# Kernel tuning notes

Hardware: AMD Instinct MI355X
Metric: run time of the kernel (lower is better)

The kernel has to match this reference:

```python
import jax, jax.numpy as jnp
import numpy as np

N_NODES = 100000
N_EDGES = 1000000
IN_DIM = 64
HID = 64
OUT = 64
NEG_SLOPE = 0.2  # PyG GATConv default


def setup_inputs() -> dict:
    key = jax.random.key(0)
    ks = jax.random.split(key, 10)
    x = jax.random.normal(ks[0], (N_NODES, IN_DIM), dtype=jnp.float32)
    edge_index = jax.random.randint(ks[1], (2, N_EDGES), 0, N_NODES, dtype=jnp.int64)
    s = 1.0 / np.sqrt(IN_DIM)
    sh = 1.0 / np.sqrt(HID)
    W_src = jax.random.uniform(ks[2], (IN_DIM, HID), jnp.float32, -s, s)
    W_dst = jax.random.uniform(ks[3], (IN_DIM, HID), jnp.float32, -s, s)
    att_src = jax.random.uniform(ks[4], (HID,), jnp.float32, -sh, sh)
    att_dst = jax.random.uniform(ks[5], (HID,), jnp.float32, -sh, sh)
    bias = jnp.zeros((HID,), jnp.float32)
    W_lin = jax.random.uniform(ks[6], (HID, OUT), jnp.float32, -sh, sh)
    b_lin = jax.random.uniform(ks[7], (OUT,), jnp.float32, -sh, sh)
    return {"x": x, "edge_index": edge_index, "W_src": W_src, "W_dst": W_dst,
            "att_src": att_src, "att_dst": att_dst, "bias": bias,
            "W_lin": W_lin, "b_lin": b_lin}


def reference(x, edge_index, W_src, W_dst, att_src, att_dst, bias, W_lin, b_lin):
    src, tgt = edge_index[0], edge_index[1]
    # Bias-free linear projections (PyG GATConv with tuple in_channels)
    h_src = x @ W_src                      # [N, HID]
    h_dst = x @ W_dst                      # [N, HID]
    a_src = h_src @ att_src                # [N]
    a_dst = h_dst @ att_dst                # [N]
    # Per-edge attention logits: LeakyReLU(a_src[j] + a_dst[i])
    e = a_src[src] + a_dst[tgt]            # [E]
    e = jnp.where(e > 0, e, NEG_SLOPE * e)
    # Segment-softmax over incoming edges of each target node
    seg_max = jax.ops.segment_max(e, tgt, num_segments=N_NODES)  # [N]
    expw = jnp.exp(e - seg_max[tgt])                             # [E]
    denom = jax.ops.segment_sum(expw, tgt, num_segments=N_NODES)  # [N]
    alpha = expw / (denom[tgt] + 1e-16)                          # [E]
    # Scatter-aggregate weighted source features
    msgs = alpha[:, None] * h_src[src]                           # [E, HID]
    out = jax.ops.segment_sum(msgs, tgt, num_segments=N_NODES)   # [N, HID]
    out = out + bias
    # Final linear + ReLU
    return jax.nn.relu(out @ W_lin + b_lin)
```

## Files before the change

kernel.cpp:

```cpp
#include <hip/hip_runtime.h>
#include <hip/hip_fp16.h>
#include <math.h>

#define HID 64
#define CBITS 6
#define CSZ 64
#define MAXB 2048
#define CAP 832
#define CAPH 576
#define PB 896
#define MSB 256

__device__ __forceinline__ float4 f4fma(float a, const float4 b, float4 c) {
    c.x = fmaf(a, b.x, c.x); c.y = fmaf(a, b.y, c.y);
    c.z = fmaf(a, b.z, c.z); c.w = fmaf(a, b.w, c.w);
    return c;
}

__global__ void init_kernel(const float* __restrict__ W_dst,
                            const float* __restrict__ att_dst,
                            float* __restrict__ vdst,
                            int* __restrict__ gcursor, int nbc) {
    if (blockIdx.x == 0 && threadIdx.x < HID) {
        int k = threadIdx.x;
        float acc = 0.0f;
#pragma unroll 8
        for (int h = 0; h < HID; ++h) acc = fmaf(W_dst[k * HID + h], att_dst[h], acc);
        vdst[k] = acc;
    }
    int stride = gridDim.x * blockDim.x;
    for (int i = blockIdx.x * blockDim.x + threadIdx.x; i < nbc; i += stride)
        gcursor[i] = i * CAP;
}

__global__ void __launch_bounds__(256)
mid_kernel(const float* __restrict__ x,
           const float* __restrict__ W_src,
           const float* __restrict__ att_src,
           const float* __restrict__ vdst,
           __half* __restrict__ h_half,
           float* __restrict__ a_src,
           float* __restrict__ a_dst, int N,
           const int* __restrict__ src, const int* __restrict__ tgt,
           int* __restrict__ gcursor, int* __restrict__ rec, int E, int nbc) {
    __shared__ __align__(16) char smraw[25088];
    const int t = threadIdx.x;

    if (blockIdx.x < PB) {
        float4* Ws4  = (float4*)smraw;
        float4* att4 = Ws4 + HID * 16;
        float4* vd4  = att4 + 16;
        float*  xs   = (float*)(vd4 + 16);

        for (int i = t; i < HID * 16; i += 256) Ws4[i] = ((const float4*)W_src)[i];
        if (t < 16) {
            att4[t] = ((const float4*)att_src)[t];
            vd4[t]  = ((const float4*)vdst)[t];
        }

        const int g0 = t >> 4;
        const int s = t & 15;
        const float4* x4 = (const float4*)x;
        uint2* h2 = (uint2*)h_half;
        float4* xs4 = (float4*)xs;

        for (int base = blockIdx.x * 32; base < N; base += PB * 32) {
            __syncthreads();
#pragma unroll
            for (int u = 0; u < 2; ++u) {
                int f = t + u * 256;
                int node = base + (f >> 4);
                xs4[f] = (node < N) ? x4[(long long)node * 16 + (f & 15)]
                                    : make_float4(0, 0, 0, 0);
            }
            __syncthreads();

            const float* xr0 = xs + g0 * HID;
            const float* xr1 = xs + (g0 + 16) * HID;

            float4 acc0 = make_float4(0, 0, 0, 0);
            float4 acc1 = make_float4(0, 0, 0, 0);
#pragma unroll 4
            for (int k = 0; k < HID; ++k) {
                float4 w = Ws4[k * 16 + s];
                acc0 = f4fma(xr0[k], w, acc0);
                acc1 = f4fma(xr1[k], w, acc1);
            }

            float4 av = att4[s], qv = vd4[s];
            float p0 = acc0.x * av.x + acc0.y * av.y + acc0.z * av.z + acc0.w * av.w;
            float p1 = acc1.x * av.x + acc1.y * av.y + acc1.z * av.z + acc1.w * av.w;
            float q0 = xr0[4 * s] * qv.x + xr0[4 * s + 1] * qv.y +
                       xr0[4 * s + 2] * qv.z + xr0[4 * s + 3] * qv.w;
            float q1 = xr1[4 * s] * qv.x + xr1[4 * s + 1] * qv.y +
                       xr1[4 * s + 2] * qv.z + xr1[4 * s + 3] * qv.w;
#pragma unroll
            for (int off = 1; off < 16; off <<= 1) {
                p0 += __shfl_xor(p0, off, 64);
                p1 += __shfl_xor(p1, off, 64);
                q0 += __shfl_xor(q0, off, 64);
                q1 += __shfl_xor(q1, off, 64);
            }

            int n0 = base + g0, n1 = base + g0 + 16;
            if (n0 < N) {
                __half2 lo = __float22half2_rn(make_float2(acc0.x, acc0.y));
                __half2 hi = __float22half2_rn(make_float2(acc0.z, acc0.w));
                uint2 pk; pk.x = *(unsigned*)&lo; pk.y = *(unsigned*)&hi;
                h2[(long long)n0 * 16 + s] = pk;
                if (s == 0) { a_src[n0] = p0; a_dst[n0] = q0; }
            }
            if (n1 < N) {
                __half2 lo = __float22half2_rn(make_float2(acc1.x, acc1.y));
                __half2 hi = __float22half2_rn(make_float2(acc1.z, acc1.w));
                uint2 pk; pk.x = *(unsigned*)&lo; pk.y = *(unsigned*)&hi;
                h2[(long long)n1 * 16 + s] = pk;
                if (s == 0) { a_src[n1] = p1; a_dst[n1] = q1; }
            }
        }
    } else {
        int* lh = (int*)smraw;
        const int bid = blockIdx.x - PB;

        for (int i = t; i < nbc; i += 256) lh[i] = 0;
        __syncthreads();
        int chunk = (E + MSB - 1) / MSB;
        int e0 = bid * chunk;
        int e1 = min(E, e0 + chunk);
        for (int e = e0 + t; e < e1; e += 256)
            atomicAdd(&lh[tgt[e] >> CBITS], 1);
        __syncthreads();
        for (int i = t; i < nbc; i += 256)
            if (lh[i]) lh[i] = atomicAdd(&gcursor[i], lh[i]);
        __syncthreads();
        for (int e = e0 + t; e < e1; e += 256) {
            int s = src[e], tg = tgt[e];
            int bi = tg >> CBITS;
            int pos = atomicAdd(&lh[bi], 1);
            if (pos < (bi + 1) * CAP)
                rec[pos] = (s << CBITS) | (tg & (CSZ - 1));
        }
    }
}

__global__ void __launch_bounds__(256)
sort_gather_kernel(const int* __restrict__ gcursor, const int* __restrict__ rec,
                   const __half* __restrict__ h_half,
                   const float* __restrict__ a_src, const float* __restrict__ a_dst,
                   const float* __restrict__ bias,
                   const float* __restrict__ W_lin, const float* __restrict__ b_lin,
                   float* __restrict__ out, int N) {
    __shared__ float4 Wl4[HID * 16];
    __shared__ float4 bs4[16], bl4[16];
    __shared__ int ssort[CAPH];
    __shared__ int hist[32];
    __shared__ int loff[33];
    __shared__ int cur[32];
    __shared__ int sd[32];

    const int t = threadIdx.x;
    for (int i = t; i < HID * 16; i += 256) Wl4[i] = ((const float4*)W_lin)[i];
    if (t < 16) {
        bs4[t] = ((const float4*)bias)[t];
        bl4[t] = ((const float4*)b_lin)[t];
    }

    const int bk = blockIdx.x >> 1;
    const int half = blockIdx.x & 1;
    const int node0 = (bk << CBITS) + half * 32;
    const int nn = min(32, N - node0);
    const int beg = bk * CAP;
    int cnt = gcursor[bk] - beg;
    if (cnt > CAP) cnt = CAP;

    if (t < 32) hist[t] = 0;
    __syncthreads();
    for (int j = t; j < cnt; j += 256) {
        int tl = rec[beg + j] & (CSZ - 1);
        if ((tl >> 5) == half) atomicAdd(&hist[tl & 31], 1);
    }
    __syncthreads();
    if (t < 32) sd[t] = hist[t];
    __syncthreads();
    for (int off = 1; off < 32; off <<= 1) {
        int v = (t < 32 && t >= off) ? sd[t - off] : 0;
        __syncthreads();
        if (t < 32) sd[t] += v;
        __syncthreads();
    }
    if (t < 32) {
        int e = sd[t] - hist[t];
        loff[t] = e; cur[t] = e;
        if (t == 31) loff[32] = min(sd[31], CAPH);
    }
    __syncthreads();
    for (int j = t; j < cnt; j += 256) {
        int r = rec[beg + j];
        int tl = r & (CSZ - 1);
        if ((tl >> 5) == half) {
            int pos = atomicAdd(&cur[tl & 31], 1);
            if (pos < CAPH) ssort[pos] = r >> CBITS;
        }
    }
    __syncthreads();

    const int lane = t & 63;
    const int w = t >> 6;
    const int g = lane >> 4;
    const int s = lane & 15;
    const int gbase = g << 4;
    const uint2* h2 = (const uint2*)h_half;
    float4* out4 = (float4*)out;

#pragma unroll 1
    for (int r2 = 0; r2 < 2; ++r2) {
        int nloc = w * 8 + r2 * 4 + g;
        int n = node0 + nloc;
        bool act = (nloc < nn);
        float adn = act ? a_dst[n] : 0.0f;
        int jb = min(loff[nloc], CAPH);
        int je = min(loff[nloc + 1], CAPH);

        float4 acc = make_float4(0, 0, 0, 0);
        float dsum = 0.0f;
        int j = jb;
        for (; j + 4 <= je; j += 4) {
            int s0 = ssort[j], s1 = ssort[j + 1], s2 = ssort[j + 2], s3 = ssort[j + 3];
            uint2 r0 = h2[(long long)s0 * 16 + s];
            uint2 r1 = h2[(long long)s1 * 16 + s];
            uint2 r2v = h2[(long long)s2 * 16 + s];
            uint2 r3 = h2[(long long)s3 * 16 + s];
            float v0 = a_src[s0] + adn, v1 = a_src[s1] + adn;
            float v2 = a_src[s2] + adn, v3 = a_src[s3] + adn;
            v0 = (v0 > 0.0f) ? v0 : 0.2f * v0;
            v1 = (v1 > 0.0f) ? v1 : 0.2f * v1;
            v2 = (v2 > 0.0f) ? v2 : 0.2f * v2;
            v3 = (v3 > 0.0f) ? v3 : 0.2f * v3;
            float w0 = __expf(v0), w1 = __expf(v1);
            float w2 = __expf(v2), w3 = __expf(v3);
            dsum += (w0 + w1) + (w2 + w3);
            float2 f0a = __half22float2(*(const __half2*)&r0.x);
            float2 f0b = __half22float2(*(const __half2*)&r0.y);
            float2 f1a = __half22float2(*(const __half2*)&r1.x);
            float2 f1b = __half22float2(*(const __half2*)&r1.y);
            float2 f2a = __half22float2(*(const __half2*)&r2v.x);
            float2 f2b = __half22float2(*(const __half2*)&r2v.y);
            float2 f3a = __half22float2(*(const __half2*)&r3.x);
            float2 f3b = __half22float2(*(const __half2*)&r3.y);
            acc.x = fmaf(w0, f0a.x, fmaf(w1, f1a.x, fmaf(w2, f2a.x, fmaf(w3, f3a.x, acc.x))));
            acc.y = fmaf(w0, f0a.y, fmaf(w1, f1a.y, fmaf(w2, f2a.y, fmaf(w3, f3a.y, acc.y))));
            acc.z = fmaf(w0, f0b.x, fmaf(w1, f1b.x, fmaf(w2, f2b.x, fmaf(w3, f3b.x, acc.z))));
            acc.w = fmaf(w0, f0b.y, fmaf(w1, f1b.y, fmaf(w2, f2b.y, fmaf(w3, f3b.y, acc.w))));
        }
        for (; j < je; ++j) {
            int s0 = ssort[j];
            uint2 r0 = h2[(long long)s0 * 16 + s];
            float v0 = a_src[s0] + adn;
            v0 = (v0 > 0.0f) ? v0 : 0.2f * v0;
            float w0 = __expf(v0);
            dsum += w0;
            float2 f0a = __half22float2(*(const __half2*)&r0.x);
            float2 f0b = __half22float2(*(const __half2*)&r0.y);
            acc.x = fmaf(w0, f0a.x, acc.x);
            acc.y = fmaf(w0, f0a.y, acc.y);
            acc.z = fmaf(w0, f0b.x, acc.z);
            acc.w = fmaf(w0, f0b.y, acc.w);
        }

        float inv = 1.0f / (dsum + 1e-16f);
        float4 bsv = bs4[s];
        float4 r;
        r.x = fmaf(acc.x, inv, bsv.x);
        r.y = fmaf(acc.y, inv, bsv.y);
        r.z = fmaf(acc.z, inv, bsv.z);
        r.w = fmaf(acc.w, inv, bsv.w);

        float4 o = bl4[s];
#pragma unroll 4
        for (int ks = 0; ks < 16; ++ks) {
            float rx = __shfl(r.x, gbase + ks, 64);
            float ry = __shfl(r.y, gbase + ks, 64);
            float rz = __shfl(r.z, gbase + ks, 64);
            float rw = __shfl(r.w, gbase + ks, 64);
            o = f4fma(rx, Wl4[(4 * ks + 0) * 16 + s], o);
            o = f4fma(ry, Wl4[(4 * ks + 1) * 16 + s], o);
            o = f4fma(rz, Wl4[(4 * ks + 2) * 16 + s], o);
            o = f4fma(rw, Wl4[(4 * ks + 3) * 16 + s], o);
        }

        if (act) {
            float4 res;
            res.x = o.x > 0.0f ? o.x : 0.0f;
            res.y = o.y > 0.0f ? o.y : 0.0f;
            res.z = o.z > 0.0f ? o.z : 0.0f;
            res.w = o.w > 0.0f ? o.w : 0.0f;
            out4[(long long)n * 16 + s] = res;
        }
    }
}

extern "C" void kernel_launch(void* const* d_in, const int* in_sizes, int n_in,
                              void* d_out, int out_size, void* d_ws, size_t ws_size,
                              hipStream_t stream) {
    const float* x       = (const float*)d_in[0];
    const int*   edge    = (const int*)d_in[1];
    const float* W_src   = (const float*)d_in[2];
    const float* W_dst   = (const float*)d_in[3];
    const float* att_src = (const float*)d_in[4];
    const float* att_dst = (const float*)d_in[5];
    const float* bias    = (const float*)d_in[6];
    const float* W_lin   = (const float*)d_in[7];
    const float* b_lin   = (const float*)d_in[8];
    float* out = (float*)d_out;

    const int N = in_sizes[0] / HID;
    const int E = in_sizes[1] / 2;
    const int* src = edge;
    const int* tgt = edge + E;
    const int nbc = (N + CSZ - 1) / CSZ;

    __half* h_half  = (__half*)d_ws;
    float*  a_src   = (float*)(h_half + (size_t)N * HID);
    float*  a_dst   = a_src + N;
    float*  vdst    = a_dst + N;
    int*    gcursor = (int*)(vdst + 64);
    int*    rec     = gcursor + MAXB;

    init_kernel<<<8, 256, 0, stream>>>(W_dst, att_dst, vdst, gcursor, nbc);
    mid_kernel<<<PB + MSB, 256, 0, stream>>>(x, W_src, att_src, vdst, h_half,
                                             a_src, a_dst, N,
                                             src, tgt, gcursor, rec, E, nbc);
    sort_gather_kernel<<<nbc * 2, 256, 0, stream>>>(gcursor, rec, h_half, a_src, a_dst,
                                                    bias, W_lin, b_lin, out, N);
}
```

Baseline: 164.3 us.

## Replace per-node sort with LDS atomic accumulation over unsorted bucket edges

The gather stage no longer sorts each bucket's edges by target node. One 512-thread block per 64-node bucket now walks the unsorted edge records and adds weighted features and exp sums into a shared-memory accumulator with atomics. This removes the histogram, prefix-scan and scatter passes and their barriers, and lets reads of the record array be vectorised. The cost is many shared-memory float atomics, with possible contention when several edges hit the same target. The W_src layout in mid_kernel is also permuted to match a strided column order.

New measurement: 527.6 us. 221% more time.

```diff
diff --git a/kernel.cpp b/kernel.cpp
--- a/kernel.cpp
+++ b/kernel.cpp
@@ -7,7 +7,6 @@
 #define CSZ 64
 #define MAXB 2048
 #define CAP 832
-#define CAPH 576
 #define PB 896
 #define MSB 256
 
@@ -52,9 +51,14 @@
         float4* vd4  = att4 + 16;
         float*  xs   = (float*)(vd4 + 16);
 
-        for (int i = t; i < HID * 16; i += 256) Ws4[i] = ((const float4*)W_src)[i];
+        for (int i = t; i < HID * 16; i += 256) {
+            int k = i >> 4, sc = i & 15;
+            const float* wr = W_src + k * HID + sc;
+            Ws4[i] = make_float4(wr[0], wr[16], wr[32], wr[48]);
+        }
         if (t < 16) {
-            att4[t] = ((const float4*)att_src)[t];
+            att4[t] = make_float4(att_src[t], att_src[t + 16],
+                                  att_src[t + 32], att_src[t + 48]);
             vd4[t]  = ((const float4*)vdst)[t];
         }
 
@@ -143,131 +147,131 @@
     }
 }
 
-__global__ void __launch_bounds__(256)
-sort_gather_kernel(const int* __restrict__ gcursor, const int* __restrict__ rec,
-                   const __half* __restrict__ h_half,
-                   const float* __restrict__ a_src, const float* __restrict__ a_dst,
-                   const float* __restrict__ bias,
-                   const float* __restrict__ W_lin, const float* __restrict__ b_lin,
-                   float* __restrict__ out, int N) {
+__global__ void __launch_bounds__(512, 8)
+gather_kernel(const int* __restrict__ gcursor, const int* __restrict__ rec,
+              const __half* __restrict__ h_half,
+              const float* __restrict__ a_src, const float* __restrict__ a_dst,
+              const float* __restrict__ bias,
+              const float* __restrict__ W_lin, const float* __restrict__ b_lin,
+              float* __restrict__ out, int N) {
     __shared__ float4 Wl4[HID * 16];
     __shared__ float4 bs4[16], bl4[16];
-    __shared__ int ssort[CAPH];
-    __shared__ int hist[32];
-    __shared__ int loff[33];
-    __shared__ int cur[32];
-    __shared__ int sd[32];
+    __shared__ __align__(16) float lacc[CSZ * HID];
+    __shared__ float ldsum[CSZ];
+    __shared__ float ladst[CSZ];
 
     const int t = threadIdx.x;
-    for (int i = t; i < HID * 16; i += 256) Wl4[i] = ((const float4*)W_lin)[i];
+    for (int i = t; i < HID * 16; i += 512) Wl4[i] = ((const float4*)W_lin)[i];
     if (t < 16) {
         bs4[t] = ((const float4*)bias)[t];
         bl4[t] = ((const float4*)b_lin)[t];
     }
-
-    const int bk = blockIdx.x >> 1;
-    const int half = blockIdx.x & 1;
-    const int node0 = (bk << CBITS) + half * 32;
-    const int nn = min(32, N - node0);
+    const int bk = blockIdx.x;
+    const int node0 = bk << CBITS;
+    for (int i = t; i < CSZ * HID; i += 512) lacc[i] = 0.0f;
+    if (t < CSZ) {
+        int n = node0 + t;
+        ldsum[t] = 0.0f;
+        ladst[t] = (n < N) ? a_dst[n] : 0.0f;
+    }
     const int beg = bk * CAP;
     int cnt = gcursor[bk] - beg;
     if (cnt > CAP) cnt = CAP;
-
-    if (t < 32) hist[t] = 0;
     __syncthreads();
-    for (int j = t; j < cnt; j += 256) {
-        int tl = rec[beg + j] & (CSZ - 1);
-        if ((tl >> 5) == half) atomicAdd(&hist[tl & 31], 1);
+
+    const int gid = t >> 4;
+    const int s = t & 15;
+    const uint2* h2 = (const uint2*)h_half;
+
+    int chunk = ((cnt + 31) >> 5 + 0);
+    chunk = (chunk + 3) & ~3;
+    int j0 = gid * chunk;
+    int j1 = min(cnt, j0 + chunk);
+    int j = j0;
+#pragma unroll 1
+    for (; j + 4 <= j1; j += 4) {
+        int4 rr = *(const int4*)(rec + beg + j);
+        int sa = rr.x >> CBITS, ta = rr.x & (CSZ - 1);
+        int sb = rr.y >> CBITS, tb = rr.y & (CSZ - 1);
+        int sc = rr.z >> CBITS, tc = rr.z & (CSZ - 1);
+        int sd = rr.w >> CBITS, td = rr.w & (CSZ - 1);
+        uint2 r0 = h2[(long long)sa * 16 + s];
+        uint2 r1 = h2[(long long)sb * 16 + s];
+        uint2 r2 = h2[(long long)sc * 16 + s];
+        uint2 r3 = h2[(long long)sd * 16 + s];
+        float v0 = a_src[sa] + ladst[ta];
+        float v1 = a_src[sb] + ladst[tb];
+        float v2 = a_src[sc] + ladst[tc];
+        float v3 = a_src[sd] + ladst[td];
+        v0 = (v0 > 0.0f) ? v0 : 0.2f * v0;
+        v1 = (v1 > 0.0f) ? v1 : 0.2f * v1;
+        v2 = (v2 > 0.0f) ? v2 : 0.2f * v2;
+        v3 = (v3 > 0.0f) ? v3 : 0.2f * v3;
+        float w0 = __expf(v0), w1 = __expf(v1);
+        float w2 = __expf(v2), w3 = __expf(v3);
+        float2 f0a = __half22float2(*(const __half2*)&r0.x);
+        float2 f0b = __half22float2(*(const __half2*)&r0.y);
+        float2 f1a = __half22float2(*(const __half2*)&r1.x);
+        float2 f1b = __half22float2(*(const __half2*)&r1.y);
+        float2 f2a = __half22float2(*(const __half2*)&r2.x);
+        float2 f2b = __half22float2(*(const __half2*)&r2.y);
+        float2 f3a = __half22float2(*(const __half2*)&r3.x);
+        float2 f3b = __half22float2(*(const __half2*)&r3.y);
+        float* p0 = lacc + ta * HID + s;
+        float* p1 = lacc + tb * HID + s;
+        float* p2 = lacc + tc * HID + s;
+        float* p3 = lacc + td * HID + s;
+        atomicAdd(p0 +  0, w0 * f0a.x);
+        atomicAdd(p0 + 16, w0 * f0a.y);
+        atomicAdd(p0 + 32, w0 * f0b.x);
+        atomicAdd(p0 + 48, w0 * f0b.y);
+        atomicAdd(p1 +  0, w1 * f1a.x);
+        atomicAdd(p1 + 16, w1 * f1a.y);
+        atomicAdd(p1 + 32, w1 * f1b.x);
+        atomicAdd(p1 + 48, w1 * f1b.y);
+        atomicAdd(p2 +  0, w2 * f2a.x);
+        atomicAdd(p2 + 16, w2 * f2a.y);
+        atomicAdd(p2 + 32, w2 * f2b.x);
+        atomicAdd(p2 + 48, w2 * f2b.y);
+        atomicAdd(p3 +  0, w3 * f3a.x);
+        atomicAdd(p3 + 16, w3 * f3a.y);
+        atomicAdd(p3 + 32, w3 * f3b.x);
+        atomicAdd(p3 + 48, w3 * f3b.y);
+        if (s == 0) {
+            atomicAdd(&ldsum[ta], w0);
+            atomicAdd(&ldsum[tb], w1);
+            atomicAdd(&ldsum[tc], w2);
+            atomicAdd(&ldsum[td], w3);
+        }
+    }
+#pragma unroll 1
+    for (; j < j1; ++j) {
+        int r = rec[beg + j];
+        int sa = r >> CBITS, ta = r & (CSZ - 1);
+        uint2 r0 = h2[(long long)sa * 16 + s];
+        float v0 = a_src[sa] + ladst[ta];
+        v0 = (v0 > 0.0f) ? v0 : 0.2f * v0;
+        float w0 = __expf(v0);
+        float2 f0a = __half22float2(*(const __half2*)&r0.x);
+        float2 f0b = __half22float2(*(const __half2*)&r0.y);
+        float* p0 = lacc + ta * HID + s;
+        atomicAdd(p0 +  0, w0 * f0a.x);
+        atomicAdd(p0 + 16, w0 * f0a.y);
+        atomicAdd(p0 + 32, w0 * f0b.x);
+        atomicAdd(p0 + 48, w0 * f0b.y);
+        if (s == 0) atomicAdd(&ldsum[ta], w0);
     }
     __syncthreads();
-    if (t < 32) sd[t] = hist[t];
-    __syncthreads();
-    for (int off = 1; off < 32; off <<= 1) {
-        int v = (t < 32 && t >= off) ? sd[t - off] : 0;
-        __syncthreads();
-        if (t < 32) sd[t] += v;
-        __syncthreads();
-    }
-    if (t < 32) {
-        int e = sd[t] - hist[t];
-        loff[t] = e; cur[t] = e;
-        if (t == 31) loff[32] = min(sd[31], CAPH);
-    }
-    __syncthreads();
-    for (int j = t; j < cnt; j += 256) {
-        int r = rec[beg + j];
-        int tl = r & (CSZ - 1);
-        if ((tl >> 5) == half) {
-            int pos = atomicAdd(&cur[tl & 31], 1);
-            if (pos < CAPH) ssort[pos] = r >> CBITS;
-        }
-    }
-    __syncthreads();
 
     const int lane = t & 63;
-    const int w = t >> 6;
-    const int g = lane >> 4;
-    const int s = lane & 15;
-    const int gbase = g << 4;
-    const uint2* h2 = (const uint2*)h_half;
+    const int gbase = (lane >> 4) << 4;
     float4* out4 = (float4*)out;
-
 #pragma unroll 1
-    for (int r2 = 0; r2 < 2; ++r2) {
-        int nloc = w * 8 + r2 * 4 + g;
+    for (int rnd = 0; rnd < 2; ++rnd) {
+        int nloc = rnd * 32 + gid;
         int n = node0 + nloc;
-        bool act = (nloc < nn);
-        float adn = act ? a_dst[n] : 0.0f;
-        int jb = min(loff[nloc], CAPH);
-        int je = min(loff[nloc + 1], CAPH);
-
-        float4 acc = make_float4(0, 0, 0, 0);
-        float dsum = 0.0f;
-        int j = jb;
-        for (; j + 4 <= je; j += 4) {
-            int s0 = ssort[j], s1 = ssort[j + 1], s2 = ssort[j + 2], s3 = ssort[j + 3];
-            uint2 r0 = h2[(long long)s0 * 16 + s];
-            uint2 r1 = h2[(long long)s1 * 16 + s];
-            uint2 r2v = h2[(long long)s2 * 16 + s];
-            uint2 r3 = h2[(long long)s3 * 16 + s];
-            float v0 = a_src[s0] + adn, v1 = a_src[s1] + adn;
-            float v2 = a_src[s2] + adn, v3 = a_src[s3] + adn;
-            v0 = (v0 > 0.0f) ? v0 : 0.2f * v0;
-            v1 = (v1 > 0.0f) ? v1 : 0.2f * v1;
-            v2 = (v2 > 0.0f) ? v2 : 0.2f * v2;
-            v3 = (v3 > 0.0f) ? v3 : 0.2f * v3;
-            float w0 = __expf(v0), w1 = __expf(v1);
-            float w2 = __expf(v2), w3 = __expf(v3);
-            dsum += (w0 + w1) + (w2 + w3);
-            float2 f0a = __half22float2(*(const __half2*)&r0.x);
-            float2 f0b = __half22float2(*(const __half2*)&r0.y);
-            float2 f1a = __half22float2(*(const __half2*)&r1.x);
-            float2 f1b = __half22float2(*(const __half2*)&r1.y);
-            float2 f2a = __half22float2(*(const __half2*)&r2v.x);
-            float2 f2b = __half22float2(*(const __half2*)&r2v.y);
-            float2 f3a = __half22float2(*(const __half2*)&r3.x);
-            float2 f3b = __half22float2(*(const __half2*)&r3.y);
-            acc.x = fmaf(w0, f0a.x, fmaf(w1, f1a.x, fmaf(w2, f2a.x, fmaf(w3, f3a.x, acc.x))));
-            acc.y = fmaf(w0, f0a.y, fmaf(w1, f1a.y, fmaf(w2, f2a.y, fmaf(w3, f3a.y, acc.y))));
-            acc.z = fmaf(w0, f0b.x, fmaf(w1, f1b.x, fmaf(w2, f2b.x, fmaf(w3, f3b.x, acc.z))));
-            acc.w = fmaf(w0, f0b.y, fmaf(w1, f1b.y, fmaf(w2, f2b.y, fmaf(w3, f3b.y, acc.w))));
-        }
-        for (; j < je; ++j) {
-            int s0 = ssort[j];
-            uint2 r0 = h2[(long long)s0 * 16 + s];
-            float v0 = a_src[s0] + adn;
-            v0 = (v0 > 0.0f) ? v0 : 0.2f * v0;
-            float w0 = __expf(v0);
-            dsum += w0;
-            float2 f0a = __half22float2(*(const __half2*)&r0.x);
-            float2 f0b = __half22float2(*(const __half2*)&r0.y);
-            acc.x = fmaf(w0, f0a.x, acc.x);
-            acc.y = fmaf(w0, f0a.y, acc.y);
-            acc.z = fmaf(w0, f0b.x, acc.z);
-            acc.w = fmaf(w0, f0b.y, acc.w);
-        }
-
-        float inv = 1.0f / (dsum + 1e-16f);
+        float4 acc = *(const float4*)(lacc + nloc * HID + 4 * s);
+        float inv = 1.0f / (ldsum[nloc] + 1e-16f);
         float4 bsv = bs4[s];
         float4 r;
         r.x = fmaf(acc.x, inv, bsv.x);
@@ -288,7 +292,7 @@
             o = f4fma(rw, Wl4[(4 * ks + 3) * 16 + s], o);
         }
 
-        if (act) {
+        if (n < N) {
             float4 res;
             res.x = o.x > 0.0f ? o.x : 0.0f;
             res.y = o.y > 0.0f ? o.y : 0.0f;
@@ -330,6 +334,6 @@
     mid_kernel<<<PB + MSB, 256, 0, stream>>>(x, W_src, att_src, vdst, h_half,
                                              a_src, a_dst, N,
                                              src, tgt, gcursor, rec, E, nbc);
-    sort_gather_kernel<<<nbc * 2, 256, 0, stream>>>(gcursor, rec, h_half, a_src, a_dst,
-                                                    bias, W_lin, b_lin, out, N);
-}
+    gather_kernel<<<nbc, 512, 0, stream>>>(gcursor, rec, h_half, a_src, a_dst,
+                                           bias, W_lin, b_lin, out, N);
+}
```
